# Kernel tuning notes

Hardware: AMD Instinct MI355X
Metric: run time of the kernel (lower is better)

Reference implementation:

```python
import jax, jax.numpy as jnp
import numpy as np

N = 20000      # nodes
E = 320000     # edges (avg degree 16)
F_IN = 32      # raw node feature dim
D = 128        # GNN_EMBEDDING_DIM = out_channels per head
HEADS = 4
RNN_H = 128    # RNN_HIDDEN_DIM
NEG_SLOPE = 0.2


def setup_inputs() -> dict:
    key = jax.random.key(0)
    ks = jax.random.split(key, 16)
    s = 0.05
    return {
        "node_features": jax.random.normal(ks[0], (N, F_IN), jnp.float32),
        "hidden_state": jax.random.normal(ks[1], (1, RNN_H), jnp.float32),
        "W_enc": jax.random.normal(ks[2], (F_IN, D), jnp.float32) * s,
        "b_enc": jax.random.normal(ks[3], (D,), jnp.float32) * s,
        "W_l": jax.random.normal(ks[4], (D, HEADS * D), jnp.float32) * s,
        "b_l": jax.random.normal(ks[5], (HEADS * D,), jnp.float32) * s,
        "W_r": jax.random.normal(ks[6], (D, HEADS * D), jnp.float32) * s,
        "b_r": jax.random.normal(ks[7], (HEADS * D,), jnp.float32) * s,
        "att": jax.random.normal(ks[8], (HEADS, D), jnp.float32) * s,
        "gat_bias": jax.random.normal(ks[9], (D,), jnp.float32) * s,
        "W_ih": jax.random.normal(ks[10], (3 * RNN_H, D), jnp.float32) * s,
        "W_hh": jax.random.normal(ks[11], (3 * RNN_H, RNN_H), jnp.float32) * s,
        "b_ih": jax.random.normal(ks[12], (3 * RNN_H,), jnp.float32) * s,
        "b_hh": jax.random.normal(ks[13], (3 * RNN_H,), jnp.float32) * s,
        "edge_index": jax.random.randint(ks[14], (2, E), 0, N, jnp.int32),
    }


def reference(node_features, hidden_state, W_enc, b_enc, W_l, b_l, W_r, b_r,
              att, gat_bias, W_ih, W_hh, b_ih, b_hh, edge_index):
    n = node_features.shape[0]
    # node encoder + ReLU
    h = jax.nn.relu(node_features @ W_enc + b_enc)                 # [N, D]

    # GATv2Conv (heads=4, concat=False), add_self_loops=True, eval (no dropout)
    loop = jnp.arange(n, dtype=edge_index.dtype)
    src = jnp.concatenate([edge_index[0], loop])                   # source j
    dst = jnp.concatenate([edge_index[1], loop])                   # target i

    xl = (h @ W_l + b_l).reshape(n, HEADS, D)                      # source proj
    xr = (h @ W_r + b_r).reshape(n, HEADS, D)                      # target proj

    e = jax.nn.leaky_relu(xl[src] + xr[dst], NEG_SLOPE)            # [Et, H, C]
    logits = jnp.einsum('ehc,hc->eh', e, att)                      # [Et, H]

    # segment softmax over incoming edges of each target node
    m = jax.ops.segment_max(logits, dst, num_segments=n)           # [N, H]
    m = jnp.where(jnp.isfinite(m), m, 0.0)
    p = jnp.exp(logits - m[dst])
    denom = jax.ops.segment_sum(p, dst, num_segments=n)
    alpha = p / jnp.maximum(denom[dst], 1e-16)                     # [Et, H]

    out = jax.ops.segment_sum(xl[src] * alpha[..., None], dst, num_segments=n)
    gat = out.mean(axis=1) + gat_bias                              # [N, D]

    # agent node 0 -> GRUCell (torch gate order: r, z, n)
    x = gat[0:1]                                                   # [1, D]
    gi = x @ W_ih.T + b_ih
    gh = hidden_state @ W_hh.T + b_hh
    i_r, i_z, i_n = jnp.split(gi, 3, axis=-1)
    h_r, h_z, h_n = jnp.split(gh, 3, axis=-1)
    r = jax.nn.sigmoid(i_r + h_r)
    z = jax.nn.sigmoid(i_z + h_z)
    ng = jnp.tanh(i_n + r * h_n)
    return (1.0 - z) * ng + z * hidden_state                       # [1, RNN_H]
```

## Files before the change

kernel.cpp:

```cpp
#include <hip/hip_runtime.h>


#define NW   32
#define NS   96
#define SLOTS 8
#define CAP  40

struct KP {
    const int* ei; int E;
    const float *nf, *W_enc, *b_enc, *W_l, *b_l, *W_r, *b_r, *att, *gat_bias,
                *hprev, *W_ih, *W_hh, *b_ih, *b_hh;
    unsigned *scnt;
    float *hsslot;
    float *lgpart;
    float *xlpub;
    float *out;
};

__device__ __forceinline__ float sigm(float x) { return 1.f / (1.f + expf(-x)); }

__global__ __launch_bounds__(256) void k_scan(KP p)
{
    __shared__ __align__(16) float wenc[4096];
    __shared__ __align__(16) float nfr[(SLOTS + 1) * 32];
    __shared__ int iaux[16];
    const int t = threadIdx.x, s = blockIdx.x;
    if (t == 0) iaux[0] = 0;
    __syncthreads();
    if ((p.E & 3) == 0) {
        int nv = p.E >> 2;
        int per = (nv + NS - 1) / NS;
        int lo = s * per, hi = min(lo + per, nv);
        const int4* d4 = (const int4*)(p.ei + p.E);
        for (int base = lo; base < hi; base += 1024) {
            int4 v[4];
            #pragma unroll
            for (int k = 0; k < 4; ++k) {
                int i = base + t + k * 256;
                v[k] = (i < hi) ? d4[i] : make_int4(1, 1, 1, 1);
            }
            #pragma unroll
            for (int k = 0; k < 4; ++k) {
                int i = base + t + k * 256;
                if (v[k].x == 0 || v[k].y == 0 || v[k].z == 0 || v[k].w == 0) {
                    #pragma unroll
                    for (int c = 0; c < 4; ++c) {
                        if ((&v[k].x)[c] == 0) {
                            int q = atomicAdd(&iaux[0], 1);
                            if (q < SLOTS) iaux[8 + q] = p.ei[4 * (long)i + c];
                        }
                    }
                }
            }
        }
    } else {
        int per = (p.E + NS - 1) / NS;
        long lo = (long)s * per, hi = lo + per; if (hi > p.E) hi = p.E;
        for (long i = lo + t; i < hi; i += 256) {
            if (p.ei[p.E + i] == 0) {
                int q = atomicAdd(&iaux[0], 1);
                if (q < SLOTS) iaux[8 + q] = p.ei[i];
            }
        }
    }
    for (int idx = t; idx < 1024; idx += 256)
        ((float4*)wenc)[idx] = ((const float4*)p.W_enc)[idx];
    float bev = (t < 128) ? p.b_enc[t] : 0.f;
    __syncthreads();
    int myc = min(iaux[0], SLOTS);
    int M2 = myc + (s == 0 ? 1 : 0);
    if (M2 > 0) {
        for (int idx = t; idx < M2 * 8; idx += 256) {
            int e = idx >> 3, f4 = idx & 7;
            long src = (e < myc) ? (long)iaux[8 + e] : 0L;
            ((float4*)nfr)[e * 8 + f4] =
                *(const float4*)(p.nf + src * 32 + f4 * 4);
        }
        __syncthreads();
        for (int e = 0; e < M2; ++e) {
            if (t < 128) {
                const float* x = nfr + e * 32;
                float a0 = 0, a1 = 0, a2 = 0, a3 = 0;
                #pragma unroll
                for (int k = 0; k < 32; k += 4) {
                    a0 += x[k]     * wenc[k * 128 + t];
                    a1 += x[k + 1] * wenc[(k + 1) * 128 + t];
                    a2 += x[k + 2] * wenc[(k + 2) * 128 + t];
                    a3 += x[k + 3] * wenc[(k + 3) * 128 + t];
                }
                long row = (e < myc) ? (long)(s * SLOTS + e) : (long)(NS * SLOTS);
                p.hsslot[row * 128 + t] = fmaxf(a0 + a1 + a2 + a3 + bev, 0.f);
            }
        }
    }
    if (t == 0) p.scnt[s * 16] = (unsigned)myc;
}

#define WLo  0
#define WRo  2048
#define HSo  4096
#define G_BUF (4096 + CAP * 128)

#define A_H0  0
#define A_XR  128
#define A_XRP 144
#define A_LGP 208
#define G_AUX 248

__global__ __launch_bounds__(256) void k_gemm(KP p)
{
    __shared__ __align__(16) float buf[G_BUF];
    __shared__ __align__(16) float aux[G_AUX];
    __shared__ int iaux[208];
    const int t = threadIdx.x, b = blockIdx.x;
    const int l4 = t & 15, g16 = t >> 4;
    const int j = b * 16 + l4;

    float blv = p.b_l[j], atv = p.att[j];
    float brv = (t < 16) ? p.b_r[b * 16 + t] : 0.f;
    if (t < 128) aux[A_H0 + t] = p.hsslot[(long)(NS * SLOTS) * 128 + t];
    if (t < 96) iaux[t] = (int)p.scnt[t * 16];
    for (int idx = t; idx < 512; idx += 256) {
        int row = idx >> 2, f4 = idx & 3;
        ((float4*)(buf + WLo))[idx] = *(const float4*)(p.W_l + (long)row * 512 + b * 16 + f4 * 4);
        ((float4*)(buf + WRo))[idx] = *(const float4*)(p.W_r + (long)row * 512 + b * 16 + f4 * 4);
    }
    __syncthreads();

    if (t < 64) {
        int col = t & 15, ch = t >> 4;
        float s = 0.f;
        #pragma unroll 8
        for (int cc = 0; cc < 32; ++cc) {
            int c = ch * 32 + cc;
            s += aux[A_H0 + c] * buf[WRo + c * 16 + col];
        }
        aux[A_XRP + t] = s;
    }
    __syncthreads();
    if (t < 16) aux[A_XR + t] = aux[A_XRP + t] + aux[A_XRP + 16 + t]
                              + aux[A_XRP + 32 + t] + aux[A_XRP + 48 + t] + brv;
    if (t < 64) {
        int s0 = 2 * t, s1 = 2 * t + 1;
        int c0 = (s0 < NS) ? iaux[s0] : 0;
        int c1 = (s1 < NS) ? iaux[s1] : 0;
        int sum = c0 + c1, pre = sum;
        #pragma unroll
        for (int off = 1; off < 64; off <<= 1) {
            int v = __shfl_up(pre, off);
            if (t >= off) pre += v;
        }
        int base = pre - sum;
        for (int u = 0; u < c0; ++u) { if (base < CAP - 1) iaux[104 + base] = s0 * SLOTS + u; ++base; }
        for (int u = 0; u < c1; ++u) { if (base < CAP - 1) iaux[104 + base] = s1 * SLOTS + u; ++base; }
        if (t == 63) iaux[100] = min(pre, CAP - 1);
    }
    __syncthreads();
    int Mc = iaux[100];
    int Mt = Mc + 1;

    for (int idx = t; idx < Mc * 32; idx += 256) {
        int e = idx >> 5, f4 = idx & 31;
        ((float4*)(buf + HSo))[e * 32 + f4] =
            *(const float4*)(p.hsslot + (long)iaux[104 + e] * 128 + f4 * 4);
    }
    if (t < 128) buf[HSo + Mc * 128 + t] = aux[A_H0 + t];
    __syncthreads();

    int ne = 0, el[3] = {0, 0, 0};
    for (int e = g16; e < Mt; e += 16) el[ne++] = e;
    float acc[3] = {0, 0, 0};
    #pragma unroll 4
    for (int c = 0; c < 128; c += 4) {
        float w0 = buf[WLo + c * 16 + l4],       w1 = buf[WLo + (c + 1) * 16 + l4];
        float w2 = buf[WLo + (c + 2) * 16 + l4], w3 = buf[WLo + (c + 3) * 16 + l4];
        #pragma unroll
        for (int k = 0; k < 3; ++k) {
            if (k < ne) {
                float4 h4 = *(const float4*)&buf[HSo + el[k] * 128 + c];
                acc[k] += h4.x * w0 + h4.y * w1 + h4.z * w2 + h4.w * w3;
            }
        }
    }
    {
        float xrj = aux[A_XR + l4];
        #pragma unroll
        for (int k = 0; k < 3; ++k) {
            if (k < ne) {
                int e = el[k];
                float xv = acc[k] + blv;
                p.xlpub[(long)e * 512 + j] = xv;
                float v = xv + xrj;
                v = (v > 0.f) ? v : 0.2f * v;
                float pp = v * atv;
                #pragma unroll
                for (int off = 8; off; off >>= 1) pp += __shfl_down(pp, off, 16);
                if (l4 == 0) aux[A_LGP + e] = pp;
            }
        }
    }
    __syncthreads();
    if (t < Mt) p.lgpart[b * CAP + t] = aux[A_LGP + t];
}

#define XLo  0
#define LGLo 20480
#define ALPo 21760
#define WIo  21920
#define WHo  23456
#define F_BUF 24992

#define B_HP  0
#define B_GH  128
#define B_GIB 140
#define B_GAT 152
#define B_BI  280
#define B_BHH 292
#define B_GI  304
#define F_AUX 316

__global__ __launch_bounds__(256) void k_final(KP p)
{
    __shared__ __align__(16) float buf[F_BUF];
    __shared__ __align__(16) float aux[F_AUX];
    __shared__ int iaux[104];
    const int t = threadIdx.x, b = blockIdx.x;

    if (t < 128) { aux[B_HP + t] = p.hprev[t]; aux[B_GAT + t] = p.gat_bias[t]; }
    if (t >= 128 && t < 140) {
        int rr = t - 128;
        int grow = (rr >> 2) * 128 + b * 4 + (rr & 3);
        aux[B_BI + rr] = p.b_ih[grow];
        aux[B_BHH + rr] = p.b_hh[grow];
    }
    if (t < 96) iaux[t] = (int)p.scnt[t * 16];
    for (int idx = t; idx < 384; idx += 256) {
        int rr = idx >> 5, f4 = idx & 31;
        int grow = (rr >> 2) * 128 + b * 4 + (rr & 3);
        ((float4*)(buf + WIo))[idx] = *(const float4*)(p.W_ih + (long)grow * 128 + f4 * 4);
        ((float4*)(buf + WHo))[idx] = *(const float4*)(p.W_hh + (long)grow * 128 + f4 * 4);
    }
    __syncthreads();
    {
        int w = t >> 6, l = t & 63;
        #pragma unroll
        for (int i = 0; i < 3; ++i) {
            int rr = w * 3 + i;
            float2 wv = ((const float2*)&buf[WHo + rr * 128])[l];
            float pp = wv.x * aux[B_HP + 2 * l] + wv.y * aux[B_HP + 2 * l + 1];
            #pragma unroll
            for (int off = 32; off; off >>= 1) pp += __shfl_down(pp, off);
            if (l == 0) aux[B_GH + rr] = pp + aux[B_BHH + rr];
        }
    }
    {
        int w = t >> 6, l = t & 63;
        #pragma unroll
        for (int i = 0; i < 3; ++i) {
            int rr = w * 3 + i;
            float2 wv = ((const float2*)&buf[WIo + rr * 128])[l];
            float pp = wv.x * aux[B_GAT + 2 * l] + wv.y * aux[B_GAT + 2 * l + 1];
            #pragma unroll
            for (int off = 32; off; off >>= 1) pp += __shfl_down(pp, off);
            if (l == 0) aux[B_GIB + rr] = pp + aux[B_BI + rr];
        }
    }
    if (t < 64) {
        int s0 = 2 * t, s1 = 2 * t + 1;
        int c0 = (s0 < NS) ? min(iaux[s0], SLOTS) : 0;
        int c1 = (s1 < NS) ? min(iaux[s1], SLOTS) : 0;
        int sum = c0 + c1;
        #pragma unroll
        for (int off = 32; off; off >>= 1) sum += __shfl_down(sum, off);
        if (t == 0) iaux[100] = min(sum, CAP - 1);
    }
    __syncthreads();
    int Mt = iaux[100] + 1;

    for (int idx = t; idx < Mt * 128; idx += 256)
        ((float4*)(buf + XLo))[idx] = ((const float4*)p.xlpub)[idx];
    for (int idx = t; idx < 320; idx += 256)
        ((float4*)(buf + LGLo))[idx] = ((const float4*)p.lgpart)[idx];
    __syncthreads();
    if (t < 4) {
        int h = t;
        float m = -1e30f;
        for (int e = 0; e < Mt; ++e) {
            float lv = 0.f;
            #pragma unroll
            for (int q = 0; q < 8; ++q) lv += buf[LGLo + (8 * h + q) * CAP + e];
            buf[ALPo + e * 4 + h] = lv;
            m = fmaxf(m, lv);
        }
        float d = 0.f;
        for (int e = 0; e < Mt; ++e) d += expf(buf[ALPo + e * 4 + h] - m);
        float inv = 1.f / fmaxf(d, 1e-16f);
        for (int e = 0; e < Mt; ++e)
            buf[ALPo + e * 4 + h] = expf(buf[ALPo + e * 4 + h] - m) * inv;
    }
    __syncthreads();
    if (t < 128) {
        float s0 = 0, s1 = 0, s2 = 0, s3 = 0;
        for (int e = 0; e < Mt; ++e) {
            const float* al = &buf[ALPo + e * 4];
            const float* xr = &buf[XLo + e * 512];
            s0 += al[0] * xr[t];
            s1 += al[1] * xr[128 + t];
            s2 += al[2] * xr[256 + t];
            s3 += al[3] * xr[384 + t];
        }
        aux[B_GAT + t] = 0.25f * (s0 + s1 + s2 + s3);
    }
    __syncthreads();
    {
        int w = t >> 6, l = t & 63;
        #pragma unroll
        for (int i = 0; i < 3; ++i) {
            int rr = w * 3 + i;
            float2 wv = ((const float2*)&buf[WIo + rr * 128])[l];
            float pp = wv.x * aux[B_GAT + 2 * l] + wv.y * aux[B_GAT + 2 * l + 1];
            #pragma unroll
            for (int off = 32; off; off >>= 1) pp += __shfl_down(pp, off);
            if (l == 0) aux[B_GI + rr] = pp + aux[B_GIB + rr];
        }
    }
    __syncthreads();
    if (t < 4) {
        int c = b * 4 + t;
        float r = sigm(aux[B_GI + t]     + aux[B_GH + t]);
        float z = sigm(aux[B_GI + 4 + t] + aux[B_GH + 4 + t]);
        float n = tanhf(aux[B_GI + 8 + t] + r * aux[B_GH + 8 + t]);
        p.out[c] = (1.f - z) * n + z * aux[B_HP + c];
    }
}

extern "C" void kernel_launch(void* const* d_in, const int* in_sizes, int n_in,
                              void* d_out, int out_size, void* d_ws, size_t ws_size,
                              hipStream_t stream) {
    KP kp;
    kp.nf       = (const float*)d_in[0];
    kp.hprev    = (const float*)d_in[1];
    kp.W_enc    = (const float*)d_in[2];
    kp.b_enc    = (const float*)d_in[3];
    kp.W_l      = (const float*)d_in[4];
    kp.b_l      = (const float*)d_in[5];
    kp.W_r      = (const float*)d_in[6];
    kp.b_r      = (const float*)d_in[7];
    kp.att      = (const float*)d_in[8];
    kp.gat_bias = (const float*)d_in[9];
    kp.W_ih     = (const float*)d_in[10];
    kp.W_hh     = (const float*)d_in[11];
    kp.b_ih     = (const float*)d_in[12];
    kp.b_hh     = (const float*)d_in[13];
    kp.ei       = (const int*)d_in[14];
    kp.E = in_sizes[14] / 2;

    char* ws = (char*)d_ws;
    kp.scnt   = (unsigned*)(ws + 0);
    kp.hsslot = (float*)(ws + 8192);
    kp.lgpart = (float*)(ws + 401920);
    kp.xlpub  = (float*)(ws + 407040);
    kp.out    = (float*)d_out;

    k_scan <<<NS, 256, 0, stream>>>(kp);
    k_gemm <<<NW, 256, 0, stream>>>(kp);
    k_final<<<NW, 256, 0, stream>>>(kp);
}
```

Measured before the change: 104.9 us.

## Precompute GRU hidden and bias gate terms in extra scan blocks, parallelize softmax

Adds NW extra blocks to the scan kernel that compute W_hh·h_prev+b_hh and W_ih·gat_bias+b_ih ahead of time and write them to workspace. This takes those matvecs and their weight loads off the critical path of the final kernel. The edge count Mc is now published once by the gemm kernel rather than re-reduced from per-block counters. The softmax logit summation and normalization are spread across 160 threads instead of running serially in 4 threads. In exchange the scan launch is larger and a few more global round trips are added.

```diff
diff --git a/kernel.cpp b/kernel.cpp
--- a/kernel.cpp
+++ b/kernel.cpp
@@ -11,6 +11,8 @@
     const float *nf, *W_enc, *b_enc, *W_l, *b_l, *W_r, *b_r, *att, *gat_bias,
                 *hprev, *W_ih, *W_hh, *b_ih, *b_hh;
     unsigned *scnt;
+    unsigned *mtc;
+    float *ghgib;
     float *hsslot;
     float *lgpart;
     float *xlpub;
@@ -23,8 +25,53 @@
 {
     __shared__ __align__(16) float wenc[4096];
     __shared__ __align__(16) float nfr[(SLOTS + 1) * 32];
+    __shared__ __align__(16) float xaux[280];
     __shared__ int iaux[16];
     const int t = threadIdx.x, s = blockIdx.x;
+
+    if (s >= NS) {
+        int bw = s - NS;
+        if (t < 128) { xaux[t] = p.hprev[t]; xaux[128 + t] = p.gat_bias[t]; }
+        if (t >= 128 && t < 140) {
+            int rr = t - 128;
+            int grow = (rr >> 2) * 128 + bw * 4 + (rr & 3);
+            xaux[256 + rr] = p.b_ih[grow];
+            xaux[268 + rr] = p.b_hh[grow];
+        }
+        for (int idx = t; idx < 384; idx += 256) {
+            int rr = idx >> 5, f4 = idx & 31;
+            int grow = (rr >> 2) * 128 + bw * 4 + (rr & 3);
+            ((float4*)(wenc))[idx]        = *(const float4*)(p.W_ih + (long)grow * 128 + f4 * 4);
+            ((float4*)(wenc + 1536))[idx] = *(const float4*)(p.W_hh + (long)grow * 128 + f4 * 4);
+        }
+        __syncthreads();
+        {
+            int w = t >> 6, l = t & 63;
+            #pragma unroll
+            for (int i = 0; i < 3; ++i) {
+                int rr = w * 3 + i;
+                float2 wv = ((const float2*)&wenc[1536 + rr * 128])[l];
+                float pp = wv.x * xaux[2 * l] + wv.y * xaux[2 * l + 1];
+                #pragma unroll
+                for (int off = 32; off; off >>= 1) pp += __shfl_down(pp, off);
+                if (l == 0) p.ghgib[bw * 32 + rr] = pp + xaux[268 + rr];
+            }
+        }
+        {
+            int w = t >> 6, l = t & 63;
+            #pragma unroll
+            for (int i = 0; i < 3; ++i) {
+                int rr = w * 3 + i;
+                float2 wv = ((const float2*)&wenc[rr * 128])[l];
+                float pp = wv.x * xaux[128 + 2 * l] + wv.y * xaux[128 + 2 * l + 1];
+                #pragma unroll
+                for (int off = 32; off; off >>= 1) pp += __shfl_down(pp, off);
+                if (l == 0) p.ghgib[bw * 32 + 16 + rr] = pp + xaux[256 + rr];
+            }
+        }
+        return;
+    }
+
     if (t == 0) iaux[0] = 0;
     __syncthreads();
     if ((p.E & 3) == 0) {
@@ -158,6 +205,7 @@
     __syncthreads();
     int Mc = iaux[100];
     int Mt = Mc + 1;
+    if (b == 0 && t == 0) p.mtc[0] = (unsigned)Mc;
 
     for (int idx = t; idx < Mc * 32; idx += 256) {
         int e = idx >> 5, f4 = idx & 31;
@@ -207,96 +255,68 @@
 #define LGLo 20480
 #define ALPo 21760
 #define WIo  21920
-#define WHo  23456
-#define F_BUF 24992
+#define F_BUF 23456
 
 #define B_HP  0
 #define B_GH  128
 #define B_GIB 140
 #define B_GAT 152
-#define B_BI  280
-#define B_BHH 292
-#define B_GI  304
-#define F_AUX 316
+#define B_GI  280
+#define B_SM  292
+#define F_AUX 300
 
 __global__ __launch_bounds__(256) void k_final(KP p)
 {
     __shared__ __align__(16) float buf[F_BUF];
     __shared__ __align__(16) float aux[F_AUX];
-    __shared__ int iaux[104];
+    __shared__ int iaux[4];
     const int t = threadIdx.x, b = blockIdx.x;
 
-    if (t < 128) { aux[B_HP + t] = p.hprev[t]; aux[B_GAT + t] = p.gat_bias[t]; }
-    if (t >= 128 && t < 140) {
+    if (t < 128) aux[B_HP + t] = p.hprev[t];
+    if (t >= 128 && t < 152) {
         int rr = t - 128;
-        int grow = (rr >> 2) * 128 + b * 4 + (rr & 3);
-        aux[B_BI + rr] = p.b_ih[grow];
-        aux[B_BHH + rr] = p.b_hh[grow];
-    }
-    if (t < 96) iaux[t] = (int)p.scnt[t * 16];
+        float v = p.ghgib[b * 32 + ((rr < 12) ? rr : (16 + rr - 12))];
+        aux[(rr < 12) ? (B_GH + rr) : (B_GIB + rr - 12)] = v;
+    }
+    if (t == 0) iaux[0] = (int)p.mtc[0];
     for (int idx = t; idx < 384; idx += 256) {
         int rr = idx >> 5, f4 = idx & 31;
         int grow = (rr >> 2) * 128 + b * 4 + (rr & 3);
         ((float4*)(buf + WIo))[idx] = *(const float4*)(p.W_ih + (long)grow * 128 + f4 * 4);
-        ((float4*)(buf + WHo))[idx] = *(const float4*)(p.W_hh + (long)grow * 128 + f4 * 4);
-    }
-    __syncthreads();
-    {
-        int w = t >> 6, l = t & 63;
-        #pragma unroll
-        for (int i = 0; i < 3; ++i) {
-            int rr = w * 3 + i;
-            float2 wv = ((const float2*)&buf[WHo + rr * 128])[l];
-            float pp = wv.x * aux[B_HP + 2 * l] + wv.y * aux[B_HP + 2 * l + 1];
-            #pragma unroll
-            for (int off = 32; off; off >>= 1) pp += __shfl_down(pp, off);
-            if (l == 0) aux[B_GH + rr] = pp + aux[B_BHH + rr];
-        }
-    }
-    {
-        int w = t >> 6, l = t & 63;
-        #pragma unroll
-        for (int i = 0; i < 3; ++i) {
-            int rr = w * 3 + i;
-            float2 wv = ((const float2*)&buf[WIo + rr * 128])[l];
-            float pp = wv.x * aux[B_GAT + 2 * l] + wv.y * aux[B_GAT + 2 * l + 1];
-            #pragma unroll
-            for (int off = 32; off; off >>= 1) pp += __shfl_down(pp, off);
-            if (l == 0) aux[B_GIB + rr] = pp + aux[B_BI + rr];
-        }
-    }
-    if (t < 64) {
-        int s0 = 2 * t, s1 = 2 * t + 1;
-        int c0 = (s0 < NS) ? min(iaux[s0], SLOTS) : 0;
-        int c1 = (s1 < NS) ? min(iaux[s1], SLOTS) : 0;
-        int sum = c0 + c1;
-        #pragma unroll
-        for (int off = 32; off; off >>= 1) sum += __shfl_down(sum, off);
-        if (t == 0) iaux[100] = min(sum, CAP - 1);
-    }
-    __syncthreads();
-    int Mt = iaux[100] + 1;
+    }
+    __syncthreads();
+    int Mt = iaux[0] + 1;
 
     for (int idx = t; idx < Mt * 128; idx += 256)
         ((float4*)(buf + XLo))[idx] = ((const float4*)p.xlpub)[idx];
     for (int idx = t; idx < 320; idx += 256)
         ((float4*)(buf + LGLo))[idx] = ((const float4*)p.lgpart)[idx];
     __syncthreads();
+    {
+        int e = t >> 2, h = t & 3;
+        if (t < 160 && e < Mt) {
+            float lv = 0.f;
+            #pragma unroll
+            for (int q = 0; q < 8; ++q) lv += buf[LGLo + (8 * h + q) * CAP + e];
+            buf[ALPo + e * 4 + h] = lv;
+        }
+    }
+    __syncthreads();
     if (t < 4) {
         int h = t;
         float m = -1e30f;
-        for (int e = 0; e < Mt; ++e) {
-            float lv = 0.f;
-            #pragma unroll
-            for (int q = 0; q < 8; ++q) lv += buf[LGLo + (8 * h + q) * CAP + e];
-            buf[ALPo + e * 4 + h] = lv;
-            m = fmaxf(m, lv);
-        }
+        for (int e = 0; e < Mt; ++e) m = fmaxf(m, buf[ALPo + e * 4 + h]);
         float d = 0.f;
         for (int e = 0; e < Mt; ++e) d += expf(buf[ALPo + e * 4 + h] - m);
-        float inv = 1.f / fmaxf(d, 1e-16f);
-        for (int e = 0; e < Mt; ++e)
-            buf[ALPo + e * 4 + h] = expf(buf[ALPo + e * 4 + h] - m) * inv;
+        aux[B_SM + h] = m;
+        aux[B_SM + 4 + h] = 1.f / fmaxf(d, 1e-16f);
+    }
+    __syncthreads();
+    {
+        int e = t >> 2, h = t & 3;
+        if (t < 160 && e < Mt)
+            buf[ALPo + e * 4 + h] =
+                expf(buf[ALPo + e * 4 + h] - aux[B_SM + h]) * aux[B_SM + 4 + h];
     }
     __syncthreads();
     if (t < 128) {
@@ -357,12 +377,14 @@
 
     char* ws = (char*)d_ws;
     kp.scnt   = (unsigned*)(ws + 0);
+    kp.mtc    = (unsigned*)(ws + 6144);
     kp.hsslot = (float*)(ws + 8192);
     kp.lgpart = (float*)(ws + 401920);
     kp.xlpub  = (float*)(ws + 407040);
+    kp.ghgib  = (float*)(ws + 488960);
     kp.out    = (float*)d_out;
 
-    k_scan <<<NS, 256, 0, stream>>>(kp);
-    k_gemm <<<NW, 256, 0, stream>>>(kp);
-    k_final<<<NW, 256, 0, stream>>>(kp);
+    k_scan <<<NS + NW, 256, 0, stream>>>(kp);
+    k_gemm <<<NW,      256, 0, stream>>>(kp);
+    k_final<<<NW,      256, 0, stream>>>(kp);
 }
```

After: 100.1 us. -4.5%, faster.
